# Kernel tuning notes

Hardware: AMD Instinct MI355X
Metric: run time of the kernel (lower is better)

Reference implementation:

```python
import jax, jax.numpy as jnp
import numpy as np
from jax import lax

HEADS = 4
DIM = 64
GATE_HID = 16


def setup_inputs() -> dict:
    key = jax.random.key(0)
    ks = jax.random.split(key, 12)
    b, c, h, w = 2, DIM, 48, 48
    s = 0.05
    x = jax.random.normal(ks[0], (b, c, h, w), jnp.float32)
    Wqkv = jax.random.normal(ks[1], (3 * c, c), jnp.float32) * s
    bqkv = jax.random.normal(ks[2], (3 * c,), jnp.float32) * s
    Wpos = jax.random.normal(ks[3], (3 * c, 1, 3, 3), jnp.float32) * s
    bpos = jax.random.normal(ks[4], (3 * c,), jnp.float32) * s
    Wg1 = jax.random.normal(ks[5], (GATE_HID, 1), jnp.float32) * 0.5
    bg1 = jax.random.normal(ks[6], (GATE_HID,), jnp.float32) * 0.1
    Wg2 = jax.random.normal(ks[7], (1, GATE_HID), jnp.float32) * 0.5
    bg2 = jax.random.normal(ks[8], (1,), jnp.float32) * 0.1
    Wproj = jax.random.normal(ks[9], (c, c), jnp.float32) * s
    bproj = jax.random.normal(ks[10], (c,), jnp.float32) * s
    return {"x": x, "Wqkv": Wqkv, "bqkv": bqkv, "Wpos": Wpos, "bpos": bpos,
            "Wg1": Wg1, "bg1": bg1, "Wg2": Wg2, "bg2": bg2,
            "Wproj": Wproj, "bproj": bproj}


def _forward(x, Wqkv, bqkv, Wpos, bpos, Wg1, bg1, Wg2, bg2, Wproj, bproj):
    b, c, h, w = x.shape
    n = h * w
    heads = HEADS
    hd = c // heads
    scale = hd ** -0.5
    # qkv 1x1 conv then 3x3 depthwise positional conv
    qkv = jnp.einsum('bchw,oc->bohw', x, Wqkv) + bqkv[None, :, None, None]
    qkv = lax.conv_general_dilated(
        qkv, Wpos, window_strides=(1, 1), padding='SAME',
        feature_group_count=3 * c,
        dimension_numbers=('NCHW', 'OIHW', 'NCHW')) + bpos[None, :, None, None]
    q, k, v = jnp.split(qkv, 3, axis=1)

    def to_heads(t):
        # [b,c,h,w] -> [b,heads,n,hd]
        return t.reshape(b, c, n).transpose(0, 2, 1).reshape(b, n, heads, hd).transpose(0, 2, 1, 3)

    q, k, v = to_heads(q), to_heads(k), to_heads(v)
    attn = jnp.einsum('bhid,bhjd->bhij', q, k) * scale  # [b,heads,n,n]
    prob = jax.nn.softmax(attn, axis=-1)
    entropy = -(prob * jnp.log(jnp.clip(prob, 1e-12))).sum(-1).mean(-1)  # [b,heads]
    # entropy gate: sigmoid(fc2(relu(fc1(e)))) * 0.9 + 0.1
    hgate = jax.nn.relu(entropy[..., None] @ Wg1.T + bg1)  # [b,heads,16]
    ratio = jax.nn.sigmoid(hgate @ Wg2.T + bg2)[..., 0] * 0.9 + 0.1  # [b,heads]
    # dynamic per-(batch,head) top-k along rows via rank threshold
    keep = jnp.clip(jnp.ceil(ratio * n).astype(jnp.int32), 1, n)  # [b,heads]
    sorted_desc = -jnp.sort(-attn, axis=-1)  # [b,heads,n,n]
    idx = jnp.broadcast_to((keep - 1)[:, :, None, None], (b, heads, n, 1))
    thresh = jnp.take_along_axis(sorted_desc, idx, axis=-1)  # [b,heads,n,1]
    sparse = jnp.where(attn >= thresh, attn, -jnp.inf)
    p = jax.nn.softmax(sparse, axis=-1)
    out = jnp.einsum('bhij,bhjd->bhid', p, v)  # [b,heads,n,hd]
    out = out.transpose(0, 2, 1, 3).reshape(b, n, c)
    out = out @ Wproj.T + bproj
    return out.transpose(0, 2, 1).reshape(b, c, h, w)


def reference(x, Wqkv, bqkv, Wpos, bpos, Wg1, bg1, Wg2, bg2, Wproj, bproj):
    return _forward(x, Wqkv, bqkv, Wpos, bpos, Wg1, bg1, Wg2, bg2, Wproj, bproj)
```

## Files before the change

kernel.cpp:

```cpp
#include <hip/hip_runtime.h>
#include <hip/hip_fp16.h>


typedef _Float16 half8_t __attribute__((ext_vector_type(8)));
typedef float floatx4 __attribute__((ext_vector_type(4)));

#define LSTR 2328

union HU { unsigned short s; _Float16 h; };
__device__ __forceinline__ _Float16 ubits_h(unsigned short u) {
  HU c; c.s = u; return c.h;
}
__device__ __forceinline__ _Float16 key_h(unsigned k) {
  unsigned short u = (k & 0x8000u) ? (unsigned short)(k & 0x7FFFu)
                                   : (unsigned short)((~k) & 0xFFFFu);
  return ubits_h(u);
}

__global__ __launch_bounds__(256) void k_qkv(const float* __restrict__ x,
                                             const float* __restrict__ W,
                                             const float* __restrict__ bias,
                                             float* __restrict__ out,
                                             float* __restrict__ ent) {
  if (blockIdx.x == 0 && threadIdx.x < 8) ent[threadIdx.x] = 0.f;
  int blk = blockIdx.x;
  int chunk = blk % 9;
  int og = (blk / 9) % 48;
  int b = blk / (9 * 48);
  int o0 = og * 4;
  int pos = chunk * 256 + threadIdx.x;
  const float* xb = x + b * 64 * 2304 + pos;
  const float* w0 = W + (o0 + 0) * 64;
  const float* w1 = W + (o0 + 1) * 64;
  const float* w2 = W + (o0 + 2) * 64;
  const float* w3 = W + (o0 + 3) * 64;
  float a0 = bias[o0 + 0], a1 = bias[o0 + 1];
  float a2 = bias[o0 + 2], a3 = bias[o0 + 3];
#pragma unroll
  for (int c = 0; c < 64; c++) {
    float xv = xb[c * 2304];
    a0 = fmaf(w0[c], xv, a0);
    a1 = fmaf(w1[c], xv, a1);
    a2 = fmaf(w2[c], xv, a2);
    a3 = fmaf(w3[c], xv, a3);
  }
  out[(b * 192 + o0 + 0) * 2304 + pos] = a0;
  out[(b * 192 + o0 + 1) * 2304 + pos] = a1;
  out[(b * 192 + o0 + 2) * 2304 + pos] = a2;
  out[(b * 192 + o0 + 3) * 2304 + pos] = a3;
}

__global__ __launch_bounds__(256) void k_dw(const float* __restrict__ qkv,
                                            const float* __restrict__ Wpos,
                                            const float* __restrict__ bpos,
                                            _Float16* __restrict__ q2,
                                            _Float16* __restrict__ k2,
                                            _Float16* __restrict__ vt) {
  __shared__ float smem[8][384];
  int blk = blockIdx.x;
  int chunk = blk % 9;
  int half = (blk / 9) % 2;
  int sel = (blk / 18) % 3;
  int head = (blk / 54) % 4;
  int b = blk / 216;
  int chbase = sel * 64 + head * 16 + half * 8;
  int bh = b * 4 + head;
  int tid = threadIdx.x;
  int p0 = chunk * 256;
  int baserow = p0 / 48;
  int rA = min(max(baserow - 1, 0), 40);

  const float* src = qkv + (size_t)(b * 192 + chbase) * 2304;
#pragma unroll
  for (int l = 0; l < 12; l++) {
    int idx = tid + l * 256;
    int ch = idx / 384;
    int off = idx - ch * 384;
    int rr = off / 48;
    int cc = off - rr * 48;
    smem[ch][off] = src[(size_t)ch * 2304 + (rA + rr) * 48 + cc];
  }
  __syncthreads();

  int pos = p0 + tid;
  int yy = pos / 48, xx = pos - yy * 48;
  int ry = yy - rA;
  float accv[8];
#pragma unroll
  for (int d = 0; d < 8; d++) {
    const float* w = Wpos + (chbase + d) * 9;
    float a = bpos[chbase + d];
#pragma unroll
    for (int dy = -1; dy <= 1; dy++) {
      int y2 = yy + dy;
      if ((unsigned)y2 < 48u) {
#pragma unroll
        for (int dx = -1; dx <= 1; dx++) {
          int x2 = xx + dx;
          if ((unsigned)x2 < 48u)
            a = fmaf(w[(dy + 1) * 3 + (dx + 1)], smem[d][(ry + dy) * 48 + x2],
                     a);
        }
      }
    }
    accv[d] = a;
  }

  if (sel == 2) {
#pragma unroll
    for (int d = 0; d < 8; d++)
      vt[((size_t)bh * 16 + half * 8 + d) * 2304 + pos] = (_Float16)accv[d];
  } else {
    _Float16 h1[8], h2[8];
#pragma unroll
    for (int d = 0; d < 8; d++) {
      float a = (sel == 0) ? accv[d] * 0.25f : accv[d];
      h1[d] = (_Float16)a;
      h2[d] = (_Float16)(a - (float)h1[d]);
    }
    _Float16* dst = ((sel == 0) ? q2 : k2) + ((size_t)bh * 2304 + pos) * 32;
    *(uint4*)(dst + half * 8) = *(uint4*)&h1[0];
    *(uint4*)(dst + 16 + half * 8) = *(uint4*)&h2[0];
  }
}

template <bool STORE>
__global__ __launch_bounds__(256) void k_ent_t(const _Float16* __restrict__ q2,
                                               const _Float16* __restrict__ k2,
                                               float* __restrict__ ent,
                                               _Float16* __restrict__ lgH) {
  __shared__ __align__(16) _Float16 tBuf[4][16][72];
  __shared__ float sWv[4][16], uWv[4][16];

  int blk = blockIdx.x;
  int rowtile = blk % 144;
  int bh = blk / 144;
  int row0 = rowtile * 16;
  int tid = threadIdx.x, lane = tid & 63, wave = tid >> 6;
  int m16 = lane & 15, quad = lane >> 4;

  const half8_t* q2v =
      (const half8_t*)(q2 + ((size_t)bh * 2304 + row0 + m16) * 32);
  half8_t A1 = q2v[quad];
  half8_t zh = {};
  half8_t A2 = (lane < 32) ? A1 : zh;
  const half8_t* kbase = (const half8_t*)(k2 + (size_t)bh * 2304 * 32);

  float s[4] = {0.f, 0.f, 0.f, 0.f}, u[4] = {0.f, 0.f, 0.f, 0.f};
  for (int g = 0; g < 9; g++) {
#pragma unroll
    for (int tt = 0; tt < 4; tt++) {
      int t = g * 4 + tt;
      int col = wave * 576 + t * 16 + m16;
      const half8_t* kk = kbase + (size_t)col * 4;
      half8_t b1 = kk[quad & 1];
      half8_t b2 = kk[2 + (quad & 1)];
      floatx4 acc = {};
      acc = __builtin_amdgcn_mfma_f32_16x16x32_f16(A2, b2, acc, 0, 0, 0);
      acc = __builtin_amdgcn_mfma_f32_16x16x32_f16(A1, b1, acc, 0, 0, 0);
#pragma unroll
      for (int i = 0; i < 4; i++) {
        if (STORE) tBuf[wave][quad * 4 + i][tt * 16 + m16] = (_Float16)acc[i];
        float e = __expf(acc[i]);
        s[i] += e;
        u[i] = fmaf(acc[i], e, u[i]);
      }
    }
    if (STORE) {
      __syncthreads();
      int rb = lane >> 3, seg = lane & 7;
#pragma unroll
      for (int it = 0; it < 2; it++) {
        int rr = it * 8 + rb;
        uint4 vv = *(const uint4*)&tBuf[wave][rr][seg * 8];
        *(uint4*)(lgH + ((size_t)bh * 2304 + row0 + rr) * 2304 + wave * 576 +
                  g * 64 + seg * 8) = vv;
      }
      __syncthreads();
    }
  }
#pragma unroll
  for (int off = 1; off < 16; off <<= 1) {
#pragma unroll
    for (int i = 0; i < 4; i++) {
      s[i] += __shfl_xor(s[i], off);
      u[i] += __shfl_xor(u[i], off);
    }
  }
  if (m16 == 0) {
#pragma unroll
    for (int i = 0; i < 4; i++) {
      sWv[wave][quad * 4 + i] = s[i];
      uWv[wave][quad * 4 + i] = u[i];
    }
  }
  __syncthreads();
  if (tid < 16) {
    float S = sWv[0][tid] + sWv[1][tid] + sWv[2][tid] + sWv[3][tid];
    float U = uWv[0][tid] + uWv[1][tid] + uWv[2][tid] + uWv[3][tid];
    float er = __logf(S) - U / S;
    er += __shfl_xor(er, 1);
    er += __shfl_xor(er, 2);
    er += __shfl_xor(er, 4);
    er += __shfl_xor(er, 8);
    if (tid == 0) atomicAdd(&ent[bh], er);
  }
}

__global__ __launch_bounds__(1024, 8) void k_attn_f(
    const _Float16* __restrict__ q2, const _Float16* __restrict__ k2,
    const _Float16* __restrict__ vt, const float* __restrict__ ent,
    const float* __restrict__ Wg1, const float* __restrict__ bg1,
    const float* __restrict__ Wg2, const float* __restrict__ bg2,
    float* __restrict__ oh) {
  __shared__ __align__(16) _Float16 lg[16 * LSTR];
  __shared__ float sS[16];

  int blk = blockIdx.x;
  int bh = blk & 7;
  int tile = blk >> 3;
  int row0 = tile * 16;
  int tid = threadIdx.x, lane = tid & 63, wave = tid >> 6;
  int m16 = lane & 15, quad = lane >> 4;

  float eAvg = ent[bh] * (1.f / 2304.f);
  float gacc = bg2[0];
#pragma unroll
  for (int i = 0; i < 16; i++) {
    float h = fmaxf(fmaf(eAvg, Wg1[i], bg1[i]), 0.f);
    gacc = fmaf(h, Wg2[i], gacc);
  }
  float ratio = 0.9f / (1.f + __expf(-gacc)) + 0.1f;
  int kp = (int)ceilf(ratio * 2304.f);
  unsigned keep = (unsigned)min(max(kp, 1), 2304);

  {
    const half8_t* q2v =
        (const half8_t*)(q2 + ((size_t)bh * 2304 + row0 + m16) * 32);
    half8_t A1 = q2v[quad];
    half8_t zh = {};
    half8_t A2 = (lane < 32) ? A1 : zh;
    const half8_t* kbase = (const half8_t*)(k2 + (size_t)bh * 2304 * 32);
#pragma unroll 3
    for (int t = 0; t < 9; t++) {
      int col = wave * 144 + t * 16 + m16;
      const half8_t* kk = kbase + (size_t)col * 4;
      half8_t b1 = kk[quad & 1];
      half8_t b2 = kk[2 + (quad & 1)];
      floatx4 acc = {};
      acc = __builtin_amdgcn_mfma_f32_16x16x32_f16(A2, b2, acc, 0, 0, 0);
      acc = __builtin_amdgcn_mfma_f32_16x16x32_f16(A1, b1, acc, 0, 0, 0);
#pragma unroll
      for (int i = 0; i < 4; i++)
        lg[(quad * 4 + i) * LSTR + col] = (_Float16)acc[i];
    }
  }
  __syncthreads();

  {
    int r = wave;
    char* rb = (char*)lg + (size_t)r * (LSTR * 2);
    const uint4* s4 = (const uint4*)rb;
    uint4 q0 = s4[lane];
    uint4 q1 = s4[lane + 64];
    uint4 q2r = s4[lane + 128];
    uint4 q3 = s4[lane + 192];
    uint2 q4 = *(const uint2*)(rb + 4096 + lane * 8);
    unsigned wb[18] = {q0.x, q0.y, q0.z, q0.w, q1.x, q1.y, q1.z, q1.w,
                       q2r.x, q2r.y, q2r.z, q2r.w, q3.x, q3.y, q3.z, q3.w,
                       q4.x, q4.y};
    unsigned ku[36];
#pragma unroll
    for (int i = 0; i < 18; i++) {
      unsigned kbi =
          wb[i] ^ (((wb[i] >> 15) & 0x00010001u) * 0x7FFFu + 0x80008000u);
      ku[2 * i + 0] = kbi & 0xFFFFu;
      ku[2 * i + 1] = kbi >> 16;
    }

    unsigned T = 0u;
    for (int bit = 15; bit >= 0; --bit) {
      unsigned cand = T | (1u << bit);
      unsigned cnt = 0u;
#pragma unroll
      for (int i = 0; i < 36; i++)
        cnt += (unsigned)__popcll(__ballot(ku[i] >= cand));
      if (cnt >= keep) {
        T = cand;
        if (cnt == keep) break;
      }
    }
    _Float16 th_h = key_h(T);

    float sp = 0.f;
    uint4* prow4 = (uint4*)rb;
#pragma unroll
    for (int g = 0; g < 4; g++) {
      uint4 o;
      unsigned ow[4];
#pragma unroll
      for (int wj = 0; wj < 4; wj++) {
        unsigned w = wb[g * 4 + wj];
        _Float16 hlo = ubits_h((unsigned short)(w & 0xFFFFu));
        _Float16 hhi = ubits_h((unsigned short)(w >> 16));
        float plo = (hlo >= th_h) ? __expf((float)hlo) : 0.f;
        float phi = (hhi >= th_h) ? __expf((float)hhi) : 0.f;
        __half2 hp = __floats2half2_rn(plo, phi);
        ow[wj] = *(unsigned*)&hp;
        if (wj == 0) sp += ((plo + phi));
      }
      o.x = ow[0]; o.y = ow[1]; o.z = ow[2]; o.w = ow[3];
      prow4[lane + g * 64] = o;
      {
        _Float16 h2a = ubits_h((unsigned short)(wb[g * 4 + 1] & 0xFFFFu));
        _Float16 h2b = ubits_h((unsigned short)(wb[g * 4 + 1] >> 16));
        _Float16 h3a = ubits_h((unsigned short)(wb[g * 4 + 2] & 0xFFFFu));
        _Float16 h3b = ubits_h((unsigned short)(wb[g * 4 + 2] >> 16));
        _Float16 h4a = ubits_h((unsigned short)(wb[g * 4 + 3] & 0xFFFFu));
        _Float16 h4b = ubits_h((unsigned short)(wb[g * 4 + 3] >> 16));
        float p2 = (h2a >= th_h) ? __expf((float)h2a) : 0.f;
        float p3 = (h2b >= th_h) ? __expf((float)h2b) : 0.f;
        float p4 = (h3a >= th_h) ? __expf((float)h3a) : 0.f;
        float p5 = (h3b >= th_h) ? __expf((float)h3b) : 0.f;
        float p6 = (h4a >= th_h) ? __expf((float)h4a) : 0.f;
        float p7 = (h4b >= th_h) ? __expf((float)h4b) : 0.f;
        sp += (p2 + p3);
        sp += (p4 + p5) + (p6 + p7);
      }
    }
    {
      _Float16 h0 = ubits_h((unsigned short)(wb[16] & 0xFFFFu));
      _Float16 h1 = ubits_h((unsigned short)(wb[16] >> 16));
      _Float16 h2 = ubits_h((unsigned short)(wb[17] & 0xFFFFu));
      _Float16 h3 = ubits_h((unsigned short)(wb[17] >> 16));
      float p0 = (h0 >= th_h) ? __expf((float)h0) : 0.f;
      float p1 = (h1 >= th_h) ? __expf((float)h1) : 0.f;
      float p2 = (h2 >= th_h) ? __expf((float)h2) : 0.f;
      float p3 = (h3 >= th_h) ? __expf((float)h3) : 0.f;
      sp += (p0 + p1) + (p2 + p3);
      uint2 o;
      __half2 hp0 = __floats2half2_rn(p0, p1); o.x = *(unsigned*)&hp0;
      __half2 hp1 = __floats2half2_rn(p2, p3); o.y = *(unsigned*)&hp1;
      *(uint2*)(rb + 4096 + lane * 8) = o;
    }
#pragma unroll
    for (int off = 1; off < 64; off <<= 1) sp += __shfl_xor(sp, off);
    if (lane == 0) sS[r] = sp;
  }
  __syncthreads();

  floatx4 acc = {};
  if (wave < 4) {
    const _Float16* vrow = vt + ((size_t)bh * 16 + m16) * 2304;
    const _Float16* prow = lg + (size_t)m16 * LSTR;
    int jb0 = wave * 576 + quad * 8;
#pragma unroll 6
    for (int t = 0; t < 18; t++) {
      int jb = jb0 + t * 32;
      half8_t a2 = *(const half8_t*)&prow[jb];
      half8_t b2 = *(const half8_t*)&vrow[jb];
      acc = __builtin_amdgcn_mfma_f32_16x16x32_f16(a2, b2, acc, 0, 0, 0);
    }
  }
  __syncthreads();
  float* red = (float*)lg;
  if (wave < 4) {
#pragma unroll
    for (int i = 0; i < 4; i++)
      red[wave * 256 + (quad * 4 + i) * 16 + m16] = acc[i];
  }
  __syncthreads();
  if (tid < 256) {
    int r = tid >> 4;
    float s2 = red[0 * 256 + tid] + red[1 * 256 + tid] +
               red[2 * 256 + tid] + red[3 * 256 + tid];
    int d = tid & 15;
    oh[((size_t)(bh * 2304 + row0 + r)) * 16 + d] = s2 / sS[r];
  }
}

__global__ __launch_bounds__(256) void k_proj(const float* __restrict__ oh,
                                              const float* __restrict__ Wp,
                                              const float* __restrict__ bp,
                                              float* __restrict__ out) {
  int blk = blockIdx.x;
  int chunk = blk % 9;
  int cog = (blk / 9) % 16;
  int b = blk / (9 * 16);
  int co0 = cog * 4;
  int pos = chunk * 256 + threadIdx.x;
  float a0 = bp[co0 + 0], a1 = bp[co0 + 1], a2 = bp[co0 + 2], a3 = bp[co0 + 3];
#pragma unroll
  for (int head = 0; head < 4; head++) {
    const float4* op =
        (const float4*)(oh + ((size_t)((b * 4 + head) * 2304 + pos)) * 16);
#pragma unroll
    for (int p = 0; p < 4; p++) {
      float4 o4 = op[p];
#pragma unroll
      for (int i = 0; i < 4; i++) {
        const float* wr = Wp + (co0 + i) * 64 + head * 16 + p * 4;
        float* ai = (i == 0) ? &a0 : ((i == 1) ? &a1 : ((i == 2) ? &a2 : &a3));
        *ai = fmaf(wr[0], o4.x, *ai);
        *ai = fmaf(wr[1], o4.y, *ai);
        *ai = fmaf(wr[2], o4.z, *ai);
        *ai = fmaf(wr[3], o4.w, *ai);
      }
    }
  }
  out[(b * 64 + co0 + 0) * 2304 + pos] = a0;
  out[(b * 64 + co0 + 1) * 2304 + pos] = a1;
  out[(b * 64 + co0 + 2) * 2304 + pos] = a2;
  out[(b * 64 + co0 + 3) * 2304 + pos] = a3;
}

extern "C" void kernel_launch(void* const* d_in, const int* in_sizes, int n_in,
                              void* d_out, int out_size, void* d_ws,
                              size_t ws_size, hipStream_t stream) {
  const float* x    = (const float*)d_in[0];
  const float* Wqkv = (const float*)d_in[1];
  const float* bqkv = (const float*)d_in[2];
  const float* Wpos = (const float*)d_in[3];
  const float* bpos = (const float*)d_in[4];
  const float* Wg1  = (const float*)d_in[5];
  const float* bg1  = (const float*)d_in[6];
  const float* Wg2  = (const float*)d_in[7];
  const float* bg2  = (const float*)d_in[8];
  const float* Wpr  = (const float*)d_in[9];
  const float* bpr  = (const float*)d_in[10];
  float* out = (float*)d_out;

  char* base = (char*)d_ws;
  float* qkv_raw = (float*)base;
  float* oh = qkv_raw + 884736;
  float* ent = oh + 294912;
  _Float16* q2 = (_Float16*)(ent + 8);
  _Float16* k2 = q2 + 589824;
  _Float16* vt = k2 + 589824;

  hipLaunchKernelGGL(k_qkv, dim3(2 * 48 * 9), dim3(256), 0, stream,
                     x, Wqkv, bqkv, qkv_raw, ent);
  hipLaunchKernelGGL(k_dw, dim3(432), dim3(256), 0, stream,
                     qkv_raw, Wpos, bpos, q2, k2, vt);
  hipLaunchKernelGGL((k_ent_t<false>), dim3(8 * 144), dim3(256), 0, stream,
                     q2, k2, ent, (_Float16*)nullptr);
  hipLaunchKernelGGL(k_attn_f, dim3(1152), dim3(1024), 0, stream,
                     q2, k2, vt, ent, Wg1, bg1, Wg2, bg2, oh);
  hipLaunchKernelGGL(k_proj, dim3(2 * 16 * 9), dim3(256), 0, stream,
                     oh, Wpr, bpr, out);
}
```

Baseline: 196.6 us.

## Fuse qkv conv into depthwise kernel, widen waves, prune top-k bit search

Merges the 1x1 qkv projection into the depthwise-conv kernel, so qkv values are computed straight into shared memory and the fp32 qkv intermediate buffer is no longer written or read. The halo rows are recomputed by neighbouring blocks in exchange. The entropy kernel moves to 1024-thread blocks with 16 waves splitting the columns and drops the unused store path. The attention kernel adds a wave-wide min/max so the radix threshold search can skip bits early, and uses 8 waves for the PV product. The projection kernel halves the output channels per block to launch more blocks.

Result: slower. 205.9 us (+4.7%).

```diff
diff --git a/kernel.cpp b/kernel.cpp
--- a/kernel.cpp
+++ b/kernel.cpp
@@ -17,77 +17,48 @@
   return ubits_h(u);
 }
 
-__global__ __launch_bounds__(256) void k_qkv(const float* __restrict__ x,
-                                             const float* __restrict__ W,
-                                             const float* __restrict__ bias,
-                                             float* __restrict__ out,
-                                             float* __restrict__ ent) {
+__global__ __launch_bounds__(256) void k_qd(
+    const float* __restrict__ x, const float* __restrict__ Wq,
+    const float* __restrict__ bq, const float* __restrict__ Wpos,
+    const float* __restrict__ bpos, _Float16* __restrict__ q2,
+    _Float16* __restrict__ k2, _Float16* __restrict__ vt,
+    float* __restrict__ ent) {
+  __shared__ float smem[4][384];
   if (blockIdx.x == 0 && threadIdx.x < 8) ent[threadIdx.x] = 0.f;
   int blk = blockIdx.x;
   int chunk = blk % 9;
-  int og = (blk / 9) % 48;
-  int b = blk / (9 * 48);
-  int o0 = og * 4;
-  int pos = chunk * 256 + threadIdx.x;
-  const float* xb = x + b * 64 * 2304 + pos;
-  const float* w0 = W + (o0 + 0) * 64;
-  const float* w1 = W + (o0 + 1) * 64;
-  const float* w2 = W + (o0 + 2) * 64;
-  const float* w3 = W + (o0 + 3) * 64;
-  float a0 = bias[o0 + 0], a1 = bias[o0 + 1];
-  float a2 = bias[o0 + 2], a3 = bias[o0 + 3];
-#pragma unroll
-  for (int c = 0; c < 64; c++) {
-    float xv = xb[c * 2304];
-    a0 = fmaf(w0[c], xv, a0);
-    a1 = fmaf(w1[c], xv, a1);
-    a2 = fmaf(w2[c], xv, a2);
-    a3 = fmaf(w3[c], xv, a3);
-  }
-  out[(b * 192 + o0 + 0) * 2304 + pos] = a0;
-  out[(b * 192 + o0 + 1) * 2304 + pos] = a1;
-  out[(b * 192 + o0 + 2) * 2304 + pos] = a2;
-  out[(b * 192 + o0 + 3) * 2304 + pos] = a3;
-}
-
-__global__ __launch_bounds__(256) void k_dw(const float* __restrict__ qkv,
-                                            const float* __restrict__ Wpos,
-                                            const float* __restrict__ bpos,
-                                            _Float16* __restrict__ q2,
-                                            _Float16* __restrict__ k2,
-                                            _Float16* __restrict__ vt) {
-  __shared__ float smem[8][384];
-  int blk = blockIdx.x;
-  int chunk = blk % 9;
-  int half = (blk / 9) % 2;
-  int sel = (blk / 18) % 3;
-  int head = (blk / 54) % 4;
-  int b = blk / 216;
-  int chbase = sel * 64 + head * 16 + half * 8;
+  int qtr = (blk / 9) % 4;
+  int sel = (blk / 36) % 3;
+  int head = (blk / 108) % 4;
+  int b = blk / 432;
+  int chbase = sel * 64 + head * 16 + qtr * 4;
   int bh = b * 4 + head;
   int tid = threadIdx.x;
   int p0 = chunk * 256;
   int baserow = p0 / 48;
   int rA = min(max(baserow - 1, 0), 40);
 
-  const float* src = qkv + (size_t)(b * 192 + chbase) * 2304;
-#pragma unroll
-  for (int l = 0; l < 12; l++) {
+  const float* xb = x + (size_t)b * 64 * 2304;
+#pragma unroll
+  for (int l = 0; l < 6; l++) {
     int idx = tid + l * 256;
     int ch = idx / 384;
     int off = idx - ch * 384;
-    int rr = off / 48;
-    int cc = off - rr * 48;
-    smem[ch][off] = src[(size_t)ch * 2304 + (rA + rr) * 48 + cc];
+    int pos2 = (rA + off / 48) * 48 + (off % 48);
+    const float* wr = Wq + (chbase + ch) * 64;
+    float a = bq[chbase + ch];
+#pragma unroll
+    for (int c = 0; c < 64; c++) a = fmaf(wr[c], xb[c * 2304 + pos2], a);
+    smem[ch][off] = a;
   }
   __syncthreads();
 
   int pos = p0 + tid;
   int yy = pos / 48, xx = pos - yy * 48;
   int ry = yy - rA;
-  float accv[8];
-#pragma unroll
-  for (int d = 0; d < 8; d++) {
+  float accv[4];
+#pragma unroll
+  for (int d = 0; d < 4; d++) {
     const float* w = Wpos + (chbase + d) * 9;
     float a = bpos[chbase + d];
 #pragma unroll
@@ -108,30 +79,26 @@
 
   if (sel == 2) {
 #pragma unroll
-    for (int d = 0; d < 8; d++)
-      vt[((size_t)bh * 16 + half * 8 + d) * 2304 + pos] = (_Float16)accv[d];
+    for (int d = 0; d < 4; d++)
+      vt[((size_t)bh * 16 + qtr * 4 + d) * 2304 + pos] = (_Float16)accv[d];
   } else {
-    _Float16 h1[8], h2[8];
-#pragma unroll
-    for (int d = 0; d < 8; d++) {
+    _Float16 h1[4], h2[4];
+#pragma unroll
+    for (int d = 0; d < 4; d++) {
       float a = (sel == 0) ? accv[d] * 0.25f : accv[d];
       h1[d] = (_Float16)a;
       h2[d] = (_Float16)(a - (float)h1[d]);
     }
     _Float16* dst = ((sel == 0) ? q2 : k2) + ((size_t)bh * 2304 + pos) * 32;
-    *(uint4*)(dst + half * 8) = *(uint4*)&h1[0];
-    *(uint4*)(dst + 16 + half * 8) = *(uint4*)&h2[0];
-  }
-}
-
-template <bool STORE>
-__global__ __launch_bounds__(256) void k_ent_t(const _Float16* __restrict__ q2,
+    *(uint2*)(dst + qtr * 4) = *(uint2*)&h1[0];
+    *(uint2*)(dst + 16 + qtr * 4) = *(uint2*)&h2[0];
+  }
+}
+
+__global__ __launch_bounds__(1024) void k_ent2(const _Float16* __restrict__ q2,
                                                const _Float16* __restrict__ k2,
-                                               float* __restrict__ ent,
-                                               _Float16* __restrict__ lgH) {
-  __shared__ __align__(16) _Float16 tBuf[4][16][72];
-  __shared__ float sWv[4][16], uWv[4][16];
-
+                                               float* __restrict__ ent) {
+  __shared__ float sWv[16][16], uWv[16][16];
   int blk = blockIdx.x;
   int rowtile = blk % 144;
   int bh = blk / 144;
@@ -147,36 +114,20 @@
   const half8_t* kbase = (const half8_t*)(k2 + (size_t)bh * 2304 * 32);
 
   float s[4] = {0.f, 0.f, 0.f, 0.f}, u[4] = {0.f, 0.f, 0.f, 0.f};
-  for (int g = 0; g < 9; g++) {
-#pragma unroll
-    for (int tt = 0; tt < 4; tt++) {
-      int t = g * 4 + tt;
-      int col = wave * 576 + t * 16 + m16;
-      const half8_t* kk = kbase + (size_t)col * 4;
-      half8_t b1 = kk[quad & 1];
-      half8_t b2 = kk[2 + (quad & 1)];
-      floatx4 acc = {};
-      acc = __builtin_amdgcn_mfma_f32_16x16x32_f16(A2, b2, acc, 0, 0, 0);
-      acc = __builtin_amdgcn_mfma_f32_16x16x32_f16(A1, b1, acc, 0, 0, 0);
-#pragma unroll
-      for (int i = 0; i < 4; i++) {
-        if (STORE) tBuf[wave][quad * 4 + i][tt * 16 + m16] = (_Float16)acc[i];
-        float e = __expf(acc[i]);
-        s[i] += e;
-        u[i] = fmaf(acc[i], e, u[i]);
-      }
-    }
-    if (STORE) {
-      __syncthreads();
-      int rb = lane >> 3, seg = lane & 7;
-#pragma unroll
-      for (int it = 0; it < 2; it++) {
-        int rr = it * 8 + rb;
-        uint4 vv = *(const uint4*)&tBuf[wave][rr][seg * 8];
-        *(uint4*)(lgH + ((size_t)bh * 2304 + row0 + rr) * 2304 + wave * 576 +
-                  g * 64 + seg * 8) = vv;
-      }
-      __syncthreads();
+#pragma unroll 3
+  for (int t = 0; t < 9; t++) {
+    int col = wave * 144 + t * 16 + m16;
+    const half8_t* kk = kbase + (size_t)col * 4;
+    half8_t b1 = kk[quad & 1];
+    half8_t b2 = kk[2 + (quad & 1)];
+    floatx4 acc = {};
+    acc = __builtin_amdgcn_mfma_f32_16x16x32_f16(A2, b2, acc, 0, 0, 0);
+    acc = __builtin_amdgcn_mfma_f32_16x16x32_f16(A1, b1, acc, 0, 0, 0);
+#pragma unroll
+    for (int i = 0; i < 4; i++) {
+      float e = __expf(acc[i]);
+      s[i] += e;
+      u[i] = fmaf(acc[i], e, u[i]);
     }
   }
 #pragma unroll
@@ -196,8 +147,12 @@
   }
   __syncthreads();
   if (tid < 16) {
-    float S = sWv[0][tid] + sWv[1][tid] + sWv[2][tid] + sWv[3][tid];
-    float U = uWv[0][tid] + uWv[1][tid] + uWv[2][tid] + uWv[3][tid];
+    float S = 0.f, U = 0.f;
+#pragma unroll
+    for (int w = 0; w < 16; w++) {
+      S += sWv[w][tid];
+      U += uWv[w][tid];
+    }
     float er = __logf(S) - U / S;
     er += __shfl_xor(er, 1);
     er += __shfl_xor(er, 2);
@@ -278,9 +233,23 @@
       ku[2 * i + 1] = kbi >> 16;
     }
 
+    unsigned kmx = ku[0], kmn = ku[0];
+#pragma unroll
+    for (int i = 1; i < 36; i++) {
+      kmx = max(kmx, ku[i]);
+      kmn = min(kmn, ku[i]);
+    }
+#pragma unroll
+    for (int off = 1; off < 64; off <<= 1) {
+      kmx = max(kmx, (unsigned)__shfl_xor((int)kmx, off));
+      kmn = min(kmn, (unsigned)__shfl_xor((int)kmn, off));
+    }
+
     unsigned T = 0u;
     for (int bit = 15; bit >= 0; --bit) {
       unsigned cand = T | (1u << bit);
+      if (cand > kmx) continue;
+      if (cand <= kmn) { T = cand; continue; }
       unsigned cnt = 0u;
 #pragma unroll
       for (int i = 0; i < 36; i++)
@@ -350,12 +319,12 @@
   __syncthreads();
 
   floatx4 acc = {};
-  if (wave < 4) {
+  if (wave < 8) {
     const _Float16* vrow = vt + ((size_t)bh * 16 + m16) * 2304;
     const _Float16* prow = lg + (size_t)m16 * LSTR;
-    int jb0 = wave * 576 + quad * 8;
-#pragma unroll 6
-    for (int t = 0; t < 18; t++) {
+    int jb0 = wave * 288 + quad * 8;
+#pragma unroll 3
+    for (int t = 0; t < 9; t++) {
       int jb = jb0 + t * 32;
       half8_t a2 = *(const half8_t*)&prow[jb];
       half8_t b2 = *(const half8_t*)&vrow[jb];
@@ -364,7 +333,7 @@
   }
   __syncthreads();
   float* red = (float*)lg;
-  if (wave < 4) {
+  if (wave < 8) {
 #pragma unroll
     for (int i = 0; i < 4; i++)
       red[wave * 256 + (quad * 4 + i) * 16 + m16] = acc[i];
@@ -372,8 +341,10 @@
   __syncthreads();
   if (tid < 256) {
     int r = tid >> 4;
-    float s2 = red[0 * 256 + tid] + red[1 * 256 + tid] +
-               red[2 * 256 + tid] + red[3 * 256 + tid];
+    float s2 = ((red[0 * 256 + tid] + red[1 * 256 + tid]) +
+                (red[2 * 256 + tid] + red[3 * 256 + tid])) +
+               ((red[4 * 256 + tid] + red[5 * 256 + tid]) +
+                (red[6 * 256 + tid] + red[7 * 256 + tid]));
     int d = tid & 15;
     oh[((size_t)(bh * 2304 + row0 + r)) * 16 + d] = s2 / sS[r];
   }
@@ -385,11 +356,11 @@
                                               float* __restrict__ out) {
   int blk = blockIdx.x;
   int chunk = blk % 9;
-  int cog = (blk / 9) % 16;
-  int b = blk / (9 * 16);
-  int co0 = cog * 4;
+  int cog = (blk / 9) % 32;
+  int b = blk / 288;
+  int co0 = cog * 2;
   int pos = chunk * 256 + threadIdx.x;
-  float a0 = bp[co0 + 0], a1 = bp[co0 + 1], a2 = bp[co0 + 2], a3 = bp[co0 + 3];
+  float a0 = bp[co0 + 0], a1 = bp[co0 + 1];
 #pragma unroll
   for (int head = 0; head < 4; head++) {
     const float4* op =
@@ -398,9 +369,9 @@
     for (int p = 0; p < 4; p++) {
       float4 o4 = op[p];
 #pragma unroll
-      for (int i = 0; i < 4; i++) {
+      for (int i = 0; i < 2; i++) {
         const float* wr = Wp + (co0 + i) * 64 + head * 16 + p * 4;
-        float* ai = (i == 0) ? &a0 : ((i == 1) ? &a1 : ((i == 2) ? &a2 : &a3));
+        float* ai = (i == 0) ? &a0 : &a1;
         *ai = fmaf(wr[0], o4.x, *ai);
         *ai = fmaf(wr[1], o4.y, *ai);
         *ai = fmaf(wr[2], o4.z, *ai);
@@ -410,8 +381,6 @@
   }
   out[(b * 64 + co0 + 0) * 2304 + pos] = a0;
   out[(b * 64 + co0 + 1) * 2304 + pos] = a1;
-  out[(b * 64 + co0 + 2) * 2304 + pos] = a2;
-  out[(b * 64 + co0 + 3) * 2304 + pos] = a3;
 }
 
 extern "C" void kernel_launch(void* const* d_in, const int* in_sizes, int n_in,
@@ -431,21 +400,18 @@
   float* out = (float*)d_out;
 
   char* base = (char*)d_ws;
-  float* qkv_raw = (float*)base;
-  float* oh = qkv_raw + 884736;
+  float* oh = (float*)base;
   float* ent = oh + 294912;
   _Float16* q2 = (_Float16*)(ent + 8);
   _Float16* k2 = q2 + 589824;
   _Float16* vt = k2 + 589824;
 
-  hipLaunchKernelGGL(k_qkv, dim3(2 * 48 * 9), dim3(256), 0, stream,
-                     x, Wqkv, bqkv, qkv_raw, ent);
-  hipLaunchKernelGGL(k_dw, dim3(432), dim3(256), 0, stream,
-                     qkv_raw, Wpos, bpos, q2, k2, vt);
-  hipLaunchKernelGGL((k_ent_t<false>), dim3(8 * 144), dim3(256), 0, stream,
-                     q2, k2, ent, (_Float16*)nullptr);
+  hipLaunchKernelGGL(k_qd, dim3(864), dim3(256), 0, stream,
+                     x, Wqkv, bqkv, Wpos, bpos, q2, k2, vt, ent);
+  hipLaunchKernelGGL(k_ent2, dim3(8 * 144), dim3(1024), 0, stream,
+                     q2, k2, ent);
   hipLaunchKernelGGL(k_attn_f, dim3(1152), dim3(1024), 0, stream,
                      q2, k2, vt, ent, Wg1, bg1, Wg2, bg2, oh);
-  hipLaunchKernelGGL(k_proj, dim3(2 * 16 * 9), dim3(256), 0, stream,
+  hipLaunchKernelGGL(k_proj, dim3(576), dim3(256), 0, stream,
                      oh, Wpr, bpr, out);
 }
```
